# Optimization experiments

Measured on AMD Instinct MI355X. Metric: run time of the kernel, lower is better.

Reference implementation:

```python
import jax, jax.numpy as jnp
import numpy as np

N, E, G = 50000, 640000, 16384
F_IN, H = 128, 128
EPS = 1e-5
_BN_S = 1.0 / np.sqrt(1.0 + EPS)  # BatchNorm1d eval mode: running_mean=0, running_var=1


def _forward(floats, edge_src, edge_dst, game_indices):
    (x, in_bn_g, in_bn_b, lin_W, lin_b, bn0_g, bn0_b,
     cW1, cb1, bn1_g, bn1_b, cW2, cb2, bn2_g, bn2_b, cW3, cb3, bn3_g, bn3_b,
     hW1, hb1, hbn_g, hbn_b, hW2, hb2, hW3, hb3,
     oW1, ob1, obn1_g, obn1_b, oW2, ob2, obn2_g, obn2_b, oW3, ob3) = floats
    n = x.shape[0]

    def bn(z, g, b):  # eval-mode BN with zero running mean, unit running var
        return g * (z * _BN_S) + b

    # GCN symmetric normalization with self-loops: deg_i = 1 + in_degree_i
    deg = jnp.ones((n,), x.dtype).at[edge_dst].add(1.0)
    dis = jax.lax.rsqrt(deg)
    coef = (dis[edge_src] * dis[edge_dst])[:, None]      # [E,1]
    self_coef = (dis * dis)[:, None]                      # [N,1] self-loop weight 1/deg

    def gcn(h, W, b):
        hw = h @ W                                        # [N,H]
        agg = jax.ops.segment_sum(hw[edge_src] * coef, edge_dst, num_segments=n)
        return agg + hw * self_coef + b

    h = bn(x, in_bn_g, in_bn_b)
    h = jax.nn.relu(bn(h @ lin_W + lin_b, bn0_g, bn0_b))
    h = h + jax.nn.relu(bn(gcn(h, cW1, cb1), bn1_g, bn1_b))
    h = h + jax.nn.relu(bn(gcn(h, cW2, cb2), bn2_g, bn2_b))
    h = h + jax.nn.relu(bn(gcn(h, cW3, cb3), bn3_g, bn3_b))

    xg = h[game_indices]                                  # [G,H]
    z = jnp.einsum('gf,hfo->hgo', xg, hW1) + hb1[:, None, :]
    z = jax.nn.relu(hbn_g[:, None, :] * (z * _BN_S) + hbn_b[:, None, :])
    z = jax.nn.relu(jnp.einsum('hgo,hok->hgk', z, hW2) + hb2[:, None, :])
    heads = (jnp.einsum('hgk,hko->hgo', z, hW3) + hb3[:, None, :])[:, :, 0].T  # [G,4]
    # outcome classification head -> [G,3]
    o = jax.nn.relu(bn(xg @ oW1 + ob1, obn1_g, obn1_b))
    o = jax.nn.relu(bn(o @ oW2 + ob2, obn2_g, obn2_b))
    o = o @ oW3 + ob3
    # columns: home_goals, away_goals, home_shots, away_shots, outcome_logits(3)
    return jnp.concatenate([heads, o], axis=-1)          # [G,7]


def setup_inputs() -> dict:
    key = jax.random.key(0)
    ks = iter(jax.random.split(key, 64))
    f32 = jnp.float32

    def rn(shape, s=0.05):
        return jax.random.normal(next(ks), shape, f32) * s

    H2, H4 = H // 2, H // 4
    return {
        'x': jax.random.normal(next(ks), (N, F_IN), f32),
        'edge_src': jax.random.randint(next(ks), (E,), 0, N),
        'edge_dst': jax.random.randint(next(ks), (E,), 0, N),
        'game_indices': jax.random.randint(next(ks), (G,), 0, N),
        'in_bn_g': jnp.ones((F_IN,), f32), 'in_bn_b': jnp.zeros((F_IN,), f32),
        'lin_W': rn((F_IN, H)), 'lin_b': jnp.zeros((H,), f32),
        'bn0_g': jnp.ones((H,), f32), 'bn0_b': jnp.zeros((H,), f32),
        'cW1': rn((H, H)), 'cb1': jnp.zeros((H,), f32),
        'bn1_g': jnp.ones((H,), f32), 'bn1_b': jnp.zeros((H,), f32),
        'cW2': rn((H, H)), 'cb2': jnp.zeros((H,), f32),
        'bn2_g': jnp.ones((H,), f32), 'bn2_b': jnp.zeros((H,), f32),
        'cW3': rn((H, H)), 'cb3': jnp.zeros((H,), f32),
        'bn3_g': jnp.ones((H,), f32), 'bn3_b': jnp.zeros((H,), f32),
        'hW1': rn((4, H, H2)), 'hb1': jnp.zeros((4, H2), f32),
        'hbn_g': jnp.ones((4, H2), f32), 'hbn_b': jnp.zeros((4, H2), f32),
        'hW2': rn((4, H2, H4)), 'hb2': jnp.zeros((4, H4), f32),
        'hW3': rn((4, H4, 1)), 'hb3': jnp.zeros((4, 1), f32),
        'oW1': rn((H, H2)), 'ob1': jnp.zeros((H2,), f32),
        'obn1_g': jnp.ones((H2,), f32), 'obn1_b': jnp.zeros((H2,), f32),
        'oW2': rn((H2, H4)), 'ob2': jnp.zeros((H4,), f32),
        'obn2_g': jnp.ones((H4,), f32), 'obn2_b': jnp.zeros((H4,), f32),
        'oW3': rn((H4, 3)), 'ob3': jnp.zeros((3,), f32),
    }


def reference(x, edge_src, edge_dst, game_indices, in_bn_g, in_bn_b, lin_W, lin_b,
              bn0_g, bn0_b, cW1, cb1, bn1_g, bn1_b, cW2, cb2, bn2_g, bn2_b,
              cW3, cb3, bn3_g, bn3_b, hW1, hb1, hbn_g, hbn_b, hW2, hb2, hW3, hb3,
              oW1, ob1, obn1_g, obn1_b, oW2, ob2, obn2_g, obn2_b, oW3, ob3):
    floats = (x, in_bn_g, in_bn_b, lin_W, lin_b, bn0_g, bn0_b,
              cW1, cb1, bn1_g, bn1_b, cW2, cb2, bn2_g, bn2_b, cW3, cb3, bn3_g, bn3_b,
              hW1, hb1, hbn_g, hbn_b, hW2, hb2, hW3, hb3,
              oW1, ob1, obn1_g, obn1_b, oW2, ob2, obn2_g, obn2_b, oW3, ob3)
    return _forward(floats, edge_src, edge_dst, game_indices)
```

## Files before the change

### kernel.cpp

```cpp
#include <hip/hip_runtime.h>
#include <hip/hip_bf16.h>

#define HDIM 128
static constexpr float BN_S = 0.99999500003749968751f;

typedef float f32x4 __attribute__((ext_vector_type(4)));
typedef short s16x8 __attribute__((ext_vector_type(8)));

union U128 { uint4 u; s16x8 s; };

__device__ __forceinline__ unsigned short f2bs(float f){
    union{float f; unsigned u;} c; c.f = f;
    unsigned r = c.u + 0x7fffu + ((c.u >> 16) & 1u);
    return (unsigned short)(r >> 16);
}
__device__ __forceinline__ float bs2f(unsigned short s){
    union{unsigned u; float f;} c; c.u = ((unsigned)s) << 16;
    return c.f;
}
__device__ __forceinline__ float ulo(unsigned u){ union{unsigned i; float f;} c; c.i = u << 16; return c.f; }
__device__ __forceinline__ float uhi(unsigned u){ union{unsigned i; float f;} c; c.i = u & 0xffff0000u; return c.f; }

__global__ __launch_bounds__(256) void k_prepzero(
    const float* __restrict__ linW, const float* __restrict__ cW1,
    const float* __restrict__ cW2, const float* __restrict__ cW3,
    const float* __restrict__ hW1, const float* __restrict__ oW1,
    const float* __restrict__ hW2, const float* __restrict__ oW2,
    unsigned short* __restrict__ wf, unsigned short* __restrict__ p1,
    unsigned short* __restrict__ p2, int* __restrict__ cnt, int N)
{
    int id = blockIdx.x * 256 + threadIdx.x;
    if (id < 65536){
        int mat = id >> 14;
        int el = id & 16383;
        int k = el >> 7, n = el & 127;
        const float* W = (mat == 0) ? linW : (mat == 1) ? cW1 : (mat == 2) ? cW2 : cW3;
        float v = W[k * 128 + n];
        unsigned short hs = f2bs(v);
        unsigned short ls = f2bs(v - bs2f(hs));
        int nt = n >> 4, lanen = n & 15, kc = k >> 5, quad = (k >> 3) & 3, j = k & 7;
        int lane = quad * 16 + lanen;
        size_t base = (size_t)mat * 32768;
        wf[base + (size_t)(((nt * 4 + kc) * 2 + 0) * 64 + lane) * 8 + j] = hs;
        wf[base + (size_t)(((nt * 4 + kc) * 2 + 1) * 64 + lane) * 8 + j] = ls;
    } else if (id < 65536 + 51200){
        int id1 = id - 65536;
        if (id1 < 40960){
            int j = id1 & 7, lane = (id1 >> 3) & 63, kc = (id1 >> 9) & 3, nt = (id1 >> 11) & 3, y = id1 >> 13;
            int k = kc * 32 + (lane >> 4) * 8 + j;
            int n = nt * 16 + (lane & 15);
            float w = (y < 4) ? hW1[(y * 128 + k) * 64 + n] : oW1[k * 64 + n];
            p1[id1] = f2bs(w);
        } else {
            int id2 = id1 - 40960;
            int j = id2 & 7, lane = (id2 >> 3) & 63, kc = (id2 >> 9) & 1, nt = (id2 >> 10) & 1, y = id2 >> 11;
            int k = kc * 32 + (lane >> 4) * 8 + j;
            int n = nt * 16 + (lane & 15);
            float w = (y < 4) ? hW2[(y * 64 + k) * 32 + n] : oW2[k * 32 + n];
            p2[id2] = f2bs(w);
        }
    } else {
        int z = id - (65536 + 51200);
        if (z < N) cnt[z] = 0;
    }
}

__global__ __launch_bounds__(256) void k_bsum(const int* __restrict__ cnt, int* __restrict__ bsum, int N){
    int b = blockIdx.x, t = threadIdx.x;
    int s = 0;
#pragma unroll
    for (int i = 0; i < 4; ++i){
        int idx = b * 1024 + i * 256 + t;
        if (idx < N) s += cnt[idx];
    }
    for (int off = 32; off; off >>= 1) s += __shfl_down(s, off);
    __shared__ int ws[4];
    if ((t & 63) == 0) ws[t >> 6] = s;
    __syncthreads();
    if (t == 0) bsum[b] = ws[0] + ws[1] + ws[2] + ws[3];
}

__global__ __launch_bounds__(256) void k_bscan(const int* __restrict__ bsum, int* __restrict__ bpre,
                                               int* __restrict__ rowptr, int B, int N, int E){
    __shared__ int arr[256];
    int t = threadIdx.x;
    int v = (t < B) ? bsum[t] : 0;
    arr[t] = v;
    for (int off = 1; off < 256; off <<= 1){
        __syncthreads();
        int x = (t >= off) ? arr[t - off] : 0;
        __syncthreads();
        arr[t] += x;
    }
    __syncthreads();
    if (t < B) bpre[t] = arr[t] - v;
    if (t == 0) rowptr[N] = E;
}

__global__ __launch_bounds__(1024) void k_scan3(const int* __restrict__ cnt, const int* __restrict__ bpre,
                                                int* __restrict__ rowptr, float* __restrict__ dis, int N){
    __shared__ int arr[1024];
    int b = blockIdx.x, t = threadIdx.x;
    int idx = b * 1024 + t;
    int c = (idx < N) ? cnt[idx] : 0;
    arr[t] = c;
    for (int off = 1; off < 1024; off <<= 1){
        __syncthreads();
        int x = (t >= off) ? arr[t - off] : 0;
        __syncthreads();
        arr[t] += x;
    }
    __syncthreads();
    if (idx < N){
        rowptr[idx] = bpre[b] + arr[t] - c;
        dis[idx] = rsqrtf(1.0f + (float)c);
    }
}

__device__ __forceinline__ void gemm01_tile(
    int tile, const float* __restrict__ A,
    const uint4* __restrict__ wf0, const uint4* __restrict__ wf1,
    const float* __restrict__ ing, const float* __restrict__ inb,
    const float* __restrict__ ebias, const float* __restrict__ eg, const float* __restrict__ eb,
    float* __restrict__ hout, unsigned short* __restrict__ hwout, int nrows,
    unsigned* sbuf)
{
    unsigned* sAhi = sbuf;
    unsigned* sAlo = sbuf + 64 * 68;
    int t = threadIdx.x;
    int row0 = tile * 64;
    for (int i = t; i < 2048; i += 256){
        int r = i >> 5, q = i & 31;
        int gr = row0 + r;
        float4 v = make_float4(0.f, 0.f, 0.f, 0.f);
        if (gr < nrows) v = *(const float4*)&A[(size_t)gr * 128 + q * 4];
        float4 g = *(const float4*)&ing[q * 4];
        float4 bo = *(const float4*)&inb[q * 4];
        v.x = v.x * (g.x * BN_S) + bo.x;
        v.y = v.y * (g.y * BN_S) + bo.y;
        v.z = v.z * (g.z * BN_S) + bo.z;
        v.w = v.w * (g.w * BN_S) + bo.w;
        unsigned u0 = __float_as_uint(v.x), u1 = __float_as_uint(v.y);
        unsigned u2 = __float_as_uint(v.z), u3 = __float_as_uint(v.w);
        uint2 hi = make_uint2((u0 >> 16) | (u1 & 0xffff0000u), (u2 >> 16) | (u3 & 0xffff0000u));
        unsigned short l0 = f2bs(v.x - __uint_as_float(u0 & 0xffff0000u));
        unsigned short l1 = f2bs(v.y - __uint_as_float(u1 & 0xffff0000u));
        unsigned short l2 = f2bs(v.z - __uint_as_float(u2 & 0xffff0000u));
        unsigned short l3 = f2bs(v.w - __uint_as_float(u3 & 0xffff0000u));
        uint2 lo = make_uint2((unsigned)l0 | ((unsigned)l1 << 16), (unsigned)l2 | ((unsigned)l3 << 16));
        *(uint2*)&sAhi[r * 68 + q * 2] = hi;
        *(uint2*)&sAlo[r * 68 + q * 2] = lo;
    }
    __syncthreads();

    int w = t >> 6, l = t & 63;
    int lanen = l & 15, quad = l >> 4;
    int mrow = w * 16 + lanen;
    f32x4 acc[8];
#pragma unroll
    for (int i = 0; i < 8; ++i) acc[i] = (f32x4){0.f, 0.f, 0.f, 0.f};

#pragma unroll 1
    for (int kc = 0; kc < 4; ++kc){
        U128 ahi, alo;
        ahi.u = *(const uint4*)&sAhi[mrow * 68 + kc * 16 + quad * 4];
        alo.u = *(const uint4*)&sAlo[mrow * 68 + kc * 16 + quad * 4];
        U128 whi[8];
#pragma unroll
        for (int nt = 0; nt < 8; ++nt)
            whi[nt].u = wf0[((nt * 4 + kc) * 2 + 0) * 64 + l];
#pragma unroll
        for (int nt = 0; nt < 8; ++nt)
            acc[nt] = __builtin_amdgcn_mfma_f32_16x16x32_bf16(ahi.s, whi[nt].s, acc[nt], 0, 0, 0);
#pragma unroll
        for (int nt = 0; nt < 8; ++nt)
            acc[nt] = __builtin_amdgcn_mfma_f32_16x16x32_bf16(alo.s, whi[nt].s, acc[nt], 0, 0, 0);
    }

    __syncthreads();
    float* so = (float*)sbuf;
#pragma unroll
    for (int nt = 0; nt < 8; ++nt){
        int n = nt * 16 + lanen;
        float bias = ebias[n], g = eg[n], bo = eb[n];
#pragma unroll
        for (int r = 0; r < 4; ++r){
            int row = w * 16 + quad * 4 + r;
            float v = g * ((acc[nt][r] + bias) * BN_S) + bo;
            so[row * 132 + n] = fmaxf(v, 0.f);
        }
    }
    __syncthreads();
    for (int i = t; i < 2048; i += 256){
        int row = i >> 5, c4 = (i & 31) * 4;
        int grow = row0 + row;
        if (grow < nrows)
            *(float4*)&hout[(size_t)grow * 128 + c4] = *(float4*)&so[row * 132 + c4];
    }

    f32x4 acc2[8];
#pragma unroll
    for (int i = 0; i < 8; ++i) acc2[i] = (f32x4){0.f, 0.f, 0.f, 0.f};
#pragma unroll 1
    for (int kc = 0; kc < 4; ++kc){
        float4 a0 = *(const float4*)&so[mrow * 132 + kc * 32 + quad * 8];
        float4 a1 = *(const float4*)&so[mrow * 132 + kc * 32 + quad * 8 + 4];
        U128 af;
        af.u.x = (unsigned)f2bs(a0.x) | ((unsigned)f2bs(a0.y) << 16);
        af.u.y = (unsigned)f2bs(a0.z) | ((unsigned)f2bs(a0.w) << 16);
        af.u.z = (unsigned)f2bs(a1.x) | ((unsigned)f2bs(a1.y) << 16);
        af.u.w = (unsigned)f2bs(a1.z) | ((unsigned)f2bs(a1.w) << 16);
        U128 wh[8];
#pragma unroll
        for (int nt = 0; nt < 8; ++nt)
            wh[nt].u = wf1[((nt * 4 + kc) * 2 + 0) * 64 + l];
#pragma unroll
        for (int nt = 0; nt < 8; ++nt)
            acc2[nt] = __builtin_amdgcn_mfma_f32_16x16x32_bf16(af.s, wh[nt].s, acc2[nt], 0, 0, 0);
    }
    __syncthreads();
    unsigned short* ss = (unsigned short*)sbuf;
#pragma unroll
    for (int nt = 0; nt < 8; ++nt){
        int n = nt * 16 + lanen;
#pragma unroll
        for (int r = 0; r < 4; ++r){
            int row = w * 16 + quad * 4 + r;
            ss[row * 136 + n] = f2bs(acc2[nt][r]);
        }
    }
    __syncthreads();
    for (int i = t; i < 1024; i += 256){
        int row = i >> 4, c = i & 15;
        int grow = row0 + row;
        if (grow < nrows)
            *(uint4*)&hwout[(size_t)grow * 128 + c * 8] = *(uint4*)&ss[row * 136 + c * 8];
    }
}

__global__ __launch_bounds__(256) void k_cg01(
    const float* __restrict__ x, const uint4* __restrict__ wf0, const uint4* __restrict__ wf1,
    const float* __restrict__ ing, const float* __restrict__ inb,
    const float* __restrict__ lb, const float* __restrict__ g0, const float* __restrict__ b0,
    float* __restrict__ hbuf, unsigned short* __restrict__ hwb, int nrows, int gb,
    const int* __restrict__ edst, int* __restrict__ cnt, int* __restrict__ rank, int E)
{
    __shared__ __align__(16) unsigned sbuf[64 * 136];
    int bid = blockIdx.x;
    if (bid < gb){
        gemm01_tile(bid, x, wf0, wf1, ing, inb, lb, g0, b0, hbuf, hwb, nrows, sbuf);
    } else {
        int base = (bid - gb) * 1024;
#pragma unroll
        for (int ii = 0; ii < 4; ++ii){
            int e = base + ii * 256 + threadIdx.x;
            if (e < E){
                int r = atomicAdd(&cnt[edst[e]], 1);
                rank[e] = r;
            }
        }
    }
}

__global__ __launch_bounds__(256) void k_fill(
    const int* __restrict__ esrc, const int* __restrict__ edst,
    const int* __restrict__ rowptr, const int* __restrict__ rank,
    const float* __restrict__ dis, int2* __restrict__ ipk, int E)
{
    int base = blockIdx.x * 1024;
#pragma unroll
    for (int ii = 0; ii < 4; ++ii){
        int e = base + ii * 256 + threadIdx.x;
        if (e < E){
            int s = esrc[e], d = edst[e];
            ipk[rowptr[d] + rank[e]] = make_int2(s, __float_as_int(dis[s]));
        }
    }
}

__global__ __launch_bounds__(256) void k_gemmb(
    const uint4* __restrict__ hb16, const uint4* __restrict__ wf,
    unsigned short* __restrict__ hwout, int nrows)
{
    __shared__ __align__(16) unsigned sbuf[64 * 68];
    int t = threadIdx.x;
    int row0 = blockIdx.x * 64;
    for (int i = t; i < 1024; i += 256){
        int r = i >> 4, c = i & 15;
        int gr = row0 + r;
        uint4 v = make_uint4(0u, 0u, 0u, 0u);
        if (gr < nrows) v = hb16[(size_t)gr * 16 + c];
        *(uint4*)&sbuf[r * 68 + c * 4] = v;
    }
    __syncthreads();

    int w = t >> 6, l = t & 63;
    int lanen = l & 15, quad = l >> 4;
    int mrow = w * 16 + lanen;
    f32x4 acc[8];
#pragma unroll
    for (int i = 0; i < 8; ++i) acc[i] = (f32x4){0.f, 0.f, 0.f, 0.f};
#pragma unroll 1
    for (int kc = 0; kc < 4; ++kc){
        U128 ah;
        ah.u = *(const uint4*)&sbuf[mrow * 68 + kc * 16 + quad * 4];
        U128 wh[8];
#pragma unroll
        for (int nt = 0; nt < 8; ++nt)
            wh[nt].u = wf[((nt * 4 + kc) * 2 + 0) * 64 + l];
#pragma unroll
        for (int nt = 0; nt < 8; ++nt)
            acc[nt] = __builtin_amdgcn_mfma_f32_16x16x32_bf16(ah.s, wh[nt].s, acc[nt], 0, 0, 0);
    }
    __syncthreads();
    unsigned short* ss = (unsigned short*)sbuf;
#pragma unroll
    for (int nt = 0; nt < 8; ++nt){
        int n = nt * 16 + lanen;
#pragma unroll
        for (int r = 0; r < 4; ++r){
            int row = w * 16 + quad * 4 + r;
            ss[row * 136 + n] = f2bs(acc[nt][r]);
        }
    }
    __syncthreads();
    for (int i = t; i < 1024; i += 256){
        int row = i >> 4, c = i & 15;
        int grow = row0 + row;
        if (grow < nrows)
            *(uint4*)&hwout[(size_t)grow * 128 + c * 8] = *(uint4*)&ss[row * 136 + c * 8];
    }
}

__global__ __launch_bounds__(256) void k_agg(
    const unsigned* __restrict__ hwu, float* __restrict__ h,
    const int* __restrict__ rowptr, const int2* __restrict__ ipk,
    const float* __restrict__ dis,
    const float* __restrict__ cb, const float* __restrict__ bg, const float* __restrict__ bb,
    uint4* __restrict__ hb16o, int N)
{
    int row = blockIdx.x * 4 + (threadIdx.x >> 6);
    if (row >= N) return;
    int l = threadIdx.x & 63;
    int sub = l >> 4, cg = l & 15;
    int b = rowptr[row], e = rowptr[row + 1];
    float acc[8];
#pragma unroll
    for (int i = 0; i < 8; ++i) acc[i] = 0.f;
    for (int p = b; p < e; p += 16){
        int base = p + sub * 4;
        if (base < e){
            int2 i0 = ipk[base];
            int2 i1 = (base + 1 < e) ? ipk[base + 1] : make_int2(i0.x, 0);
            int2 i2 = (base + 2 < e) ? ipk[base + 2] : make_int2(i0.x, 0);
            int2 i3 = (base + 3 < e) ? ipk[base + 3] : make_int2(i0.x, 0);
            uint4 v0 = *(const uint4*)&hwu[(size_t)i0.x * 64 + cg * 4];
            uint4 v1 = *(const uint4*)&hwu[(size_t)i1.x * 64 + cg * 4];
            uint4 v2 = *(const uint4*)&hwu[(size_t)i2.x * 64 + cg * 4];
            uint4 v3 = *(const uint4*)&hwu[(size_t)i3.x * 64 + cg * 4];
            float c0 = __int_as_float(i0.y), c1 = __int_as_float(i1.y);
            float c2 = __int_as_float(i2.y), c3 = __int_as_float(i3.y);
            acc[0] = fmaf(ulo(v0.x), c0, acc[0]); acc[1] = fmaf(uhi(v0.x), c0, acc[1]);
            acc[2] = fmaf(ulo(v0.y), c0, acc[2]); acc[3] = fmaf(uhi(v0.y), c0, acc[3]);
            acc[4] = fmaf(ulo(v0.z), c0, acc[4]); acc[5] = fmaf(uhi(v0.z), c0, acc[5]);
            acc[6] = fmaf(ulo(v0.w), c0, acc[6]); acc[7] = fmaf(uhi(v0.w), c0, acc[7]);
            acc[0] = fmaf(ulo(v1.x), c1, acc[0]); acc[1] = fmaf(uhi(v1.x), c1, acc[1]);
            acc[2] = fmaf(ulo(v1.y), c1, acc[2]); acc[3] = fmaf(uhi(v1.y), c1, acc[3]);
            acc[4] = fmaf(ulo(v1.z), c1, acc[4]); acc[5] = fmaf(uhi(v1.z), c1, acc[5]);
            acc[6] = fmaf(ulo(v1.w), c1, acc[6]); acc[7] = fmaf(uhi(v1.w), c1, acc[7]);
            acc[0] = fmaf(ulo(v2.x), c2, acc[0]); acc[1] = fmaf(uhi(v2.x), c2, acc[1]);
            acc[2] = fmaf(ulo(v2.y), c2, acc[2]); acc[3] = fmaf(uhi(v2.y), c2, acc[3]);
            acc[4] = fmaf(ulo(v2.z), c2, acc[4]); acc[5] = fmaf(uhi(v2.z), c2, acc[5]);
            acc[6] = fmaf(ulo(v2.w), c2, acc[6]); acc[7] = fmaf(uhi(v2.w), c2, acc[7]);
            acc[0] = fmaf(ulo(v3.x), c3, acc[0]); acc[1] = fmaf(uhi(v3.x), c3, acc[1]);
            acc[2] = fmaf(ulo(v3.y), c3, acc[2]); acc[3] = fmaf(uhi(v3.y), c3, acc[3]);
            acc[4] = fmaf(ulo(v3.z), c3, acc[4]); acc[5] = fmaf(uhi(v3.z), c3, acc[5]);
            acc[6] = fmaf(ulo(v3.w), c3, acc[6]); acc[7] = fmaf(uhi(v3.w), c3, acc[7]);
        }
    }
#pragma unroll
    for (int i = 0; i < 8; ++i){
        acc[i] += __shfl_xor(acc[i], 16);
        acc[i] += __shfl_xor(acc[i], 32);
    }
    if (sub == 0){
        float d = dis[row];
        float dd = d * d;
        uint4 sv = *(const uint4*)&hwu[(size_t)row * 64 + cg * 4];
        float sf[8] = {ulo(sv.x), uhi(sv.x), ulo(sv.y), uhi(sv.y),
                       ulo(sv.z), uhi(sv.z), ulo(sv.w), uhi(sv.w)};
        float4 c0 = *(const float4*)&cb[cg * 8], c1 = *(const float4*)&cb[cg * 8 + 4];
        float4 g0 = *(const float4*)&bg[cg * 8], g1 = *(const float4*)&bg[cg * 8 + 4];
        float4 b0 = *(const float4*)&bb[cg * 8], b1 = *(const float4*)&bb[cg * 8 + 4];
        float cc[8] = {c0.x, c0.y, c0.z, c0.w, c1.x, c1.y, c1.z, c1.w};
        float gg[8] = {g0.x, g0.y, g0.z, g0.w, g1.x, g1.y, g1.z, g1.w};
        float bo[8] = {b0.x, b0.y, b0.z, b0.w, b1.x, b1.y, b1.z, b1.w};
        float4 cur0 = *(float4*)&h[(size_t)row * 128 + cg * 8];
        float4 cur1 = *(float4*)&h[(size_t)row * 128 + cg * 8 + 4];
        float o[8] = {cur0.x, cur0.y, cur0.z, cur0.w, cur1.x, cur1.y, cur1.z, cur1.w};
#pragma unroll
        for (int i = 0; i < 8; ++i){
            float v = gg[i] * ((acc[i] * d + sf[i] * dd + cc[i]) * BN_S) + bo[i];
            o[i] += fmaxf(v, 0.f);
        }
        *(float4*)&h[(size_t)row * 128 + cg * 8] = make_float4(o[0], o[1], o[2], o[3]);
        *(float4*)&h[(size_t)row * 128 + cg * 8 + 4] = make_float4(o[4], o[5], o[6], o[7]);
        uint4 pk;
        pk.x = (unsigned)f2bs(o[0]) | ((unsigned)f2bs(o[1]) << 16);
        pk.y = (unsigned)f2bs(o[2]) | ((unsigned)f2bs(o[3]) << 16);
        pk.z = (unsigned)f2bs(o[4]) | ((unsigned)f2bs(o[5]) << 16);
        pk.w = (unsigned)f2bs(o[6]) | ((unsigned)f2bs(o[7]) << 16);
        hb16o[(size_t)row * 16 + cg] = pk;
    }
}

__global__ __launch_bounds__(256) void k_headmm(
    const uint4* __restrict__ hb16, const int* __restrict__ gidx,
    const uint4* __restrict__ p1v, const uint4* __restrict__ p2v,
    const float* __restrict__ hb1, const float* __restrict__ hg1, const float* __restrict__ hbb1,
    const float* __restrict__ hb2,
    const float* __restrict__ hW3, const float* __restrict__ hb3,
    const float* __restrict__ ob1, const float* __restrict__ og1, const float* __restrict__ obb1,
    const float* __restrict__ ob2, const float* __restrict__ og2, const float* __restrict__ obb2,
    const float* __restrict__ oW3, const float* __restrict__ ob3,
    float* __restrict__ out, int G)
{
    __shared__ __align__(16) unsigned sxg[64 * 68];
    __shared__ __align__(16) unsigned sz1u[64 * 36];
    __shared__ __align__(16) unsigned sz2u[64 * 20];
    __shared__ float sb1[64], sg1[64], sbb1[64];
    __shared__ float sb2[32], sg2[32], sbb2[32];
    __shared__ float sW3[96];
    __shared__ float sb3[3];
    __shared__ int sgi[64];

    int t = threadIdx.x;
    int gblk = blockIdx.x;
    int w = t >> 6, l = t & 63;
    int lanen = l & 15, quad = l >> 4;

    if (t < 64){
        int g = gblk * 64 + t;
        sgi[t] = (g < G) ? gidx[g] : 0;
    }
    __syncthreads();
    for (int i = t; i < 1024; i += 256){
        int r = i >> 4, c = i & 15;
        int node = sgi[r];
        uint4 v = hb16[(size_t)node * 16 + c];
        *(uint4*)&sxg[r * 68 + c * 4] = v;
    }

    for (int y = 0; y < 5; ++y){
        bool bn2 = (y == 4);
        const float* b1  = bn2 ? ob1  : (hb1 + y * 64);
        const float* g1  = bn2 ? og1  : (hg1 + y * 64);
        const float* bb1 = bn2 ? obb1 : (hbb1 + y * 64);
        const float* b2  = bn2 ? ob2  : (hb2 + y * 32);
        const float* W3  = bn2 ? oW3  : (hW3 + y * 32);
        const float* b3  = bn2 ? ob3  : (hb3 + y);
        int nc3 = bn2 ? 3 : 1;

        __syncthreads();
        if (t < 64){
            sb1[t] = b1[t]; sg1[t] = g1[t]; sbb1[t] = bb1[t];
            if (t < 3) sb3[t] = (t < nc3) ? b3[t] : 0.f;
        } else if (t < 96){
            int p = t - 64;
            sb2[p] = b2[p];
            sg2[p] = bn2 ? og2[p] : 1.f;
            sbb2[p] = bn2 ? obb2[p] : 0.f;
        } else if (t < 192){
            int i = t - 96;
            sW3[i] = (i < 32 * nc3) ? W3[i] : 0.f;
        }
        __syncthreads();

        f32x4 acc1[4] = {{0.f,0.f,0.f,0.f},{0.f,0.f,0.f,0.f},{0.f,0.f,0.f,0.f},{0.f,0.f,0.f,0.f}};
#pragma unroll
        for (int kc = 0; kc < 4; ++kc){
            U128 a;
            a.u = *(const uint4*)&sxg[(w * 16 + lanen) * 68 + kc * 16 + quad * 4];
#pragma unroll
            for (int nt = 0; nt < 4; ++nt){
                U128 bfr;
                bfr.u = p1v[((y * 4 + nt) * 4 + kc) * 64 + l];
                acc1[nt] = __builtin_amdgcn_mfma_f32_16x16x32_bf16(a.s, bfr.s, acc1[nt], 0, 0, 0);
            }
        }
        {
            unsigned short* sz1s = (unsigned short*)sz1u;
#pragma unroll
            for (int nt = 0; nt < 4; ++nt){
                int n = nt * 16 + lanen;
                float g = sg1[n], bia = sb1[n], bt = sbb1[n];
#pragma unroll
                for (int r = 0; r < 4; ++r){
                    int row = w * 16 + quad * 4 + r;
                    float v = g * ((acc1[nt][r] + bia) * BN_S) + bt;
                    sz1s[row * 72 + n] = f2bs(fmaxf(v, 0.f));
                }
            }
        }
        __syncthreads();

        f32x4 acc2[2] = {{0.f,0.f,0.f,0.f},{0.f,0.f,0.f,0.f}};
#pragma unroll
        for (int kc = 0; kc < 2; ++kc){
            U128 a;
            a.u = *(const uint4*)&sz1u[(w * 16 + lanen) * 36 + kc * 16 + quad * 4];
#pragma unroll
            for (int nt = 0; nt < 2; ++nt){
                U128 bfr;
                bfr.u = p2v[((y * 2 + nt) * 2 + kc) * 64 + l];
                acc2[nt] = __builtin_amdgcn_mfma_f32_16x16x32_bf16(a.s, bfr.s, acc2[nt], 0, 0, 0);
            }
        }
        {
            unsigned short* sz2s = (unsigned short*)sz2u;
#pragma unroll
            for (int nt = 0; nt < 2; ++nt){
                int n = nt * 16 + lanen;
                float bia = sb2[n], g = sg2[n], bt = sbb2[n];
#pragma unroll
                for (int r = 0; r < 4; ++r){
                    int row = w * 16 + quad * 4 + r;
                    float v = acc2[nt][r] + bia;
                    if (bn2) v = g * (v * BN_S) + bt;
                    sz2s[row * 40 + n] = f2bs(fmaxf(v, 0.f));
                }
            }
        }
        __syncthreads();

        const unsigned short* sz2s = (const unsigned short*)sz2u;
        if (!bn2){
            if (t < 64){
                int g = gblk * 64 + t;
                if (g < G){
                    float s = sb3[0];
#pragma unroll
                    for (int p = 0; p < 32; ++p) s = fmaf(bs2f(sz2s[t * 40 + p]), sW3[p], s);
                    out[(size_t)g * 7 + y] = s;
                }
            }
        } else {
            if (t < 192){
                int gl = t / 3, c = t % 3;
                int g = gblk * 64 + gl;
                if (g < G){
                    float s = sb3[c];
#pragma unroll
                    for (int p = 0; p < 32; ++p) s = fmaf(bs2f(sz2s[gl * 40 + p]), sW3[p * 3 + c], s);
                    out[(size_t)g * 7 + 4 + c] = s;
                }
            }
        }
    }
}

extern "C" void kernel_launch(void* const* d_in, const int* in_sizes, int n_in,
                              void* d_out, int out_size, void* d_ws, size_t ws_size,
                              hipStream_t stream)
{
    const float* x    = (const float*)d_in[0];
    const int* esrc   = (const int*)d_in[1];
    const int* edst   = (const int*)d_in[2];
    const int* gidx   = (const int*)d_in[3];
    const float* in_g = (const float*)d_in[4];
    const float* in_b = (const float*)d_in[5];
    const float* lin_W = (const float*)d_in[6];
    const float* lin_b = (const float*)d_in[7];
    const float* bn0_g = (const float*)d_in[8];
    const float* bn0_b = (const float*)d_in[9];
    const float* cW[3] = {(const float*)d_in[10], (const float*)d_in[14], (const float*)d_in[18]};
    const float* cb[3] = {(const float*)d_in[11], (const float*)d_in[15], (const float*)d_in[19]};
    const float* bg[3] = {(const float*)d_in[12], (const float*)d_in[16], (const float*)d_in[20]};
    const float* bb[3] = {(const float*)d_in[13], (const float*)d_in[17], (const float*)d_in[21]};
    const float* hW1 = (const float*)d_in[22];
    const float* hb1 = (const float*)d_in[23];
    const float* hg1 = (const float*)d_in[24];
    const float* hbb1 = (const float*)d_in[25];
    const float* hW2 = (const float*)d_in[26];
    const float* hb2 = (const float*)d_in[27];
    const float* hW3 = (const float*)d_in[28];
    const float* hb3 = (const float*)d_in[29];
    const float* oW1 = (const float*)d_in[30];
    const float* ob1 = (const float*)d_in[31];
    const float* og1 = (const float*)d_in[32];
    const float* obb1 = (const float*)d_in[33];
    const float* oW2 = (const float*)d_in[34];
    const float* ob2 = (const float*)d_in[35];
    const float* og2 = (const float*)d_in[36];
    const float* obb2 = (const float*)d_in[37];
    const float* oW3 = (const float*)d_in[38];
    const float* ob3 = (const float*)d_in[39];

    const int N = in_sizes[0] / HDIM;
    const int E = in_sizes[1];
    const int G = in_sizes[3];

    char* wsp = (char*)d_ws;
    size_t off = 0;
    auto alloc = [&](size_t bytes) -> char* {
        char* p = wsp + off;
        off = (off + bytes + 255) & ~(size_t)255;
        return p;
    };
    float* dis    = (float*)alloc((size_t)N * 4);
    int* rowptr   = (int*)alloc((size_t)(N + 1) * 4);
    int* cnt      = (int*)alloc((size_t)N * 4);
    int* rank     = (int*)alloc((size_t)E * 4);
    int2* ipk     = (int2*)alloc((size_t)E * 8);
    float* hbuf   = (float*)alloc((size_t)N * HDIM * 4);
    unsigned short* hwb = (unsigned short*)alloc((size_t)N * HDIM * 2);
    unsigned short* hb16 = (unsigned short*)alloc((size_t)N * HDIM * 2);
    unsigned short* p1 = (unsigned short*)alloc(40960 * 2);
    unsigned short* p2 = (unsigned short*)alloc(10240 * 2);
    unsigned short* wf = (unsigned short*)alloc((size_t)4 * 32768 * 2);
    int* bsum     = (int*)alloc(256 * 4);
    int* bpre     = (int*)alloc(256 * 4);

    int gb = (N + 63) / 64;
    int CB = (E + 1023) / 1024;
    int B = (N + 1023) / 1024;
    int prepTot = 65536 + 51200 + N;

    k_prepzero<<<dim3((prepTot + 255) / 256), dim3(256), 0, stream>>>(
        lin_W, cW[0], cW[1], cW[2], hW1, oW1, hW2, oW2, wf, p1, p2, cnt, N);
    k_cg01<<<dim3(gb + CB), dim3(256), 0, stream>>>(
        x, (const uint4*)wf, (const uint4*)(wf + (size_t)32768),
        in_g, in_b, lin_b, bn0_g, bn0_b, hbuf, hwb, N, gb, edst, cnt, rank, E);
    k_bsum<<<dim3(B), dim3(256), 0, stream>>>(cnt, bsum, N);
    k_bscan<<<dim3(1), dim3(256), 0, stream>>>(bsum, bpre, rowptr, B, N, E);
    k_scan3<<<dim3(B), dim3(1024), 0, stream>>>(cnt, bpre, rowptr, dis, N);
    k_fill<<<dim3(CB), dim3(256), 0, stream>>>(esrc, edst, rowptr, rank, dis, ipk, E);
    k_agg<<<dim3((N + 3) / 4), dim3(256), 0, stream>>>((const unsigned*)hwb, hbuf, rowptr, ipk,
                                                       dis, cb[0], bg[0], bb[0], (uint4*)hb16, N);
    for (int lyr = 1; lyr < 3; ++lyr){
        k_gemmb<<<dim3(gb), dim3(256), 0, stream>>>((const uint4*)hb16,
                                                    (const uint4*)(wf + (size_t)(1 + lyr) * 32768),
                                                    hwb, N);
        k_agg<<<dim3((N + 3) / 4), dim3(256), 0, stream>>>((const unsigned*)hwb, hbuf, rowptr, ipk,
                                                           dis, cb[lyr], bg[lyr], bb[lyr], (uint4*)hb16, N);
    }
    k_headmm<<<dim3((G + 63) / 64), dim3(256), 0, stream>>>(
        (const uint4*)hb16, gidx, (const uint4*)p1, (const uint4*)p2,
        hb1, hg1, hbb1, hb2, hW3, hb3,
        ob1, og1, obb1, ob2, og2, obb2, oW3, ob3,
        (float*)d_out, G);
}
```

Measured before the change: 364.1 us.

## Fuse GCN aggregation with next layer's GEMM via shared memory, ping-pong hw buffers

The aggregation for layers 1 and 2 now runs inside a combined kernel that keeps each 64-row block's bf16 output in shared memory and immediately multiplies it by the next layer's weights with MFMA. This removes the round trip of hb16 through global memory and two kernel launches. Because the gather reads hw while the kernel writes the next hw, two ping-pong buffers are used. The final layer's aggregation no longer writes the fp32 residual buffer, since nothing reads it afterwards. The trade-off is lower parallelism: one block now handles 64 rows instead of 4, with each wave processing 16 rows serially, which can worsen latency hiding and load balance on skewed degrees.

```diff
diff --git a/kernel.cpp b/kernel.cpp
--- a/kernel.cpp
+++ b/kernel.cpp
@@ -278,24 +278,102 @@
     }
 }
 
-__global__ __launch_bounds__(256) void k_gemmb(
-    const uint4* __restrict__ hb16, const uint4* __restrict__ wf,
-    unsigned short* __restrict__ hwout, int nrows)
+__global__ __launch_bounds__(256) void k_aggemm(
+    const unsigned* __restrict__ hwu, float* __restrict__ h,
+    const int* __restrict__ rowptr, const int2* __restrict__ ipk,
+    const float* __restrict__ dis,
+    const float* __restrict__ cb, const float* __restrict__ bg, const float* __restrict__ bb,
+    const uint4* __restrict__ wf, unsigned short* __restrict__ hwout, int N)
 {
     __shared__ __align__(16) unsigned sbuf[64 * 68];
     int t = threadIdx.x;
+    int w = t >> 6, l = t & 63;
+    int sub = l >> 4, cg = l & 15;
+    int lanen = l & 15, quad = l >> 4;
     int row0 = blockIdx.x * 64;
-    for (int i = t; i < 1024; i += 256){
-        int r = i >> 4, c = i & 15;
-        int gr = row0 + r;
-        uint4 v = make_uint4(0u, 0u, 0u, 0u);
-        if (gr < nrows) v = hb16[(size_t)gr * 16 + c];
-        *(uint4*)&sbuf[r * 68 + c * 4] = v;
-    }
-    __syncthreads();
-
-    int w = t >> 6, l = t & 63;
-    int lanen = l & 15, quad = l >> 4;
+
+    if (row0 + 64 > N){
+        for (int i = t; i < 1024; i += 256){
+            int r = i >> 4;
+            if (row0 + r >= N) *(uint4*)&sbuf[r * 68 + (i & 15) * 4] = make_uint4(0u,0u,0u,0u);
+        }
+    }
+
+    for (int rr = 0; rr < 16; ++rr){
+        int row = row0 + w * 16 + rr;
+        if (row >= N) break;
+        int b = rowptr[row], e = rowptr[row + 1];
+        float acc[8];
+#pragma unroll
+        for (int i = 0; i < 8; ++i) acc[i] = 0.f;
+        for (int p = b; p < e; p += 16){
+            int base = p + sub * 4;
+            if (base < e){
+                int2 i0 = ipk[base];
+                int2 i1 = (base + 1 < e) ? ipk[base + 1] : make_int2(i0.x, 0);
+                int2 i2 = (base + 2 < e) ? ipk[base + 2] : make_int2(i0.x, 0);
+                int2 i3 = (base + 3 < e) ? ipk[base + 3] : make_int2(i0.x, 0);
+                uint4 v0 = *(const uint4*)&hwu[(size_t)i0.x * 64 + cg * 4];
+                uint4 v1 = *(const uint4*)&hwu[(size_t)i1.x * 64 + cg * 4];
+                uint4 v2 = *(const uint4*)&hwu[(size_t)i2.x * 64 + cg * 4];
+                uint4 v3 = *(const uint4*)&hwu[(size_t)i3.x * 64 + cg * 4];
+                float c0 = __int_as_float(i0.y), c1 = __int_as_float(i1.y);
+                float c2 = __int_as_float(i2.y), c3 = __int_as_float(i3.y);
+                acc[0] = fmaf(ulo(v0.x), c0, acc[0]); acc[1] = fmaf(uhi(v0.x), c0, acc[1]);
+                acc[2] = fmaf(ulo(v0.y), c0, acc[2]); acc[3] = fmaf(uhi(v0.y), c0, acc[3]);
+                acc[4] = fmaf(ulo(v0.z), c0, acc[4]); acc[5] = fmaf(uhi(v0.z), c0, acc[5]);
+                acc[6] = fmaf(ulo(v0.w), c0, acc[6]); acc[7] = fmaf(uhi(v0.w), c0, acc[7]);
+                acc[0] = fmaf(ulo(v1.x), c1, acc[0]); acc[1] = fmaf(uhi(v1.x), c1, acc[1]);
+                acc[2] = fmaf(ulo(v1.y), c1, acc[2]); acc[3] = fmaf(uhi(v1.y), c1, acc[3]);
+                acc[4] = fmaf(ulo(v1.z), c1, acc[4]); acc[5] = fmaf(uhi(v1.z), c1, acc[5]);
+                acc[6] = fmaf(ulo(v1.w), c1, acc[6]); acc[7] = fmaf(uhi(v1.w), c1, acc[7]);
+                acc[0] = fmaf(ulo(v2.x), c2, acc[0]); acc[1] = fmaf(uhi(v2.x), c2, acc[1]);
+                acc[2] = fmaf(ulo(v2.y), c2, acc[2]); acc[3] = fmaf(uhi(v2.y), c2, acc[3]);
+                acc[4] = fmaf(ulo(v2.z), c2, acc[4]); acc[5] = fmaf(uhi(v2.z), c2, acc[5]);
+                acc[6] = fmaf(ulo(v2.w), c2, acc[6]); acc[7] = fmaf(uhi(v2.w), c2, acc[7]);
+                acc[0] = fmaf(ulo(v3.x), c3, acc[0]); acc[1] = fmaf(uhi(v3.x), c3, acc[1]);
+                acc[2] = fmaf(ulo(v3.y), c3, acc[2]); acc[3] = fmaf(uhi(v3.y), c3, acc[3]);
+                acc[4] = fmaf(ulo(v3.z), c3, acc[4]); acc[5] = fmaf(uhi(v3.z), c3, acc[5]);
+                acc[6] = fmaf(ulo(v3.w), c3, acc[6]); acc[7] = fmaf(uhi(v3.w), c3, acc[7]);
+            }
+        }
+#pragma unroll
+        for (int i = 0; i < 8; ++i){
+            acc[i] += __shfl_xor(acc[i], 16);
+            acc[i] += __shfl_xor(acc[i], 32);
+        }
+        if (sub == 0){
+            float d = dis[row];
+            float dd = d * d;
+            uint4 sv = *(const uint4*)&hwu[(size_t)row * 64 + cg * 4];
+            float sf[8] = {ulo(sv.x), uhi(sv.x), ulo(sv.y), uhi(sv.y),
+                           ulo(sv.z), uhi(sv.z), ulo(sv.w), uhi(sv.w)};
+            float4 c0 = *(const float4*)&cb[cg * 8], c1 = *(const float4*)&cb[cg * 8 + 4];
+            float4 g0 = *(const float4*)&bg[cg * 8], g1 = *(const float4*)&bg[cg * 8 + 4];
+            float4 b0 = *(const float4*)&bb[cg * 8], b1 = *(const float4*)&bb[cg * 8 + 4];
+            float cc[8] = {c0.x, c0.y, c0.z, c0.w, c1.x, c1.y, c1.z, c1.w};
+            float gg[8] = {g0.x, g0.y, g0.z, g0.w, g1.x, g1.y, g1.z, g1.w};
+            float bo[8] = {b0.x, b0.y, b0.z, b0.w, b1.x, b1.y, b1.z, b1.w};
+            float4 cur0 = *(float4*)&h[(size_t)row * 128 + cg * 8];
+            float4 cur1 = *(float4*)&h[(size_t)row * 128 + cg * 8 + 4];
+            float o[8] = {cur0.x, cur0.y, cur0.z, cur0.w, cur1.x, cur1.y, cur1.z, cur1.w};
+#pragma unroll
+            for (int i = 0; i < 8; ++i){
+                float v = gg[i] * ((acc[i] * d + sf[i] * dd + cc[i]) * BN_S) + bo[i];
+                o[i] += fmaxf(v, 0.f);
+            }
+            *(float4*)&h[(size_t)row * 128 + cg * 8] = make_float4(o[0], o[1], o[2], o[3]);
+            *(float4*)&h[(size_t)row * 128 + cg * 8 + 4] = make_float4(o[4], o[5], o[6], o[7]);
+            uint4 pk;
+            pk.x = (unsigned)f2bs(o[0]) | ((unsigned)f2bs(o[1]) << 16);
+            pk.y = (unsigned)f2bs(o[2]) | ((unsigned)f2bs(o[3]) << 16);
+            pk.z = (unsigned)f2bs(o[4]) | ((unsigned)f2bs(o[5]) << 16);
+            pk.w = (unsigned)f2bs(o[6]) | ((unsigned)f2bs(o[7]) << 16);
+            *(uint4*)&sbuf[(w * 16 + rr) * 68 + cg * 4] = pk;
+        }
+    }
+    __syncthreads();
+
     int mrow = w * 16 + lanen;
     f32x4 acc[8];
 #pragma unroll
@@ -327,13 +405,13 @@
     for (int i = t; i < 1024; i += 256){
         int row = i >> 4, c = i & 15;
         int grow = row0 + row;
-        if (grow < nrows)
+        if (grow < N)
             *(uint4*)&hwout[(size_t)grow * 128 + c * 8] = *(uint4*)&ss[row * 136 + c * 8];
     }
 }
 
-__global__ __launch_bounds__(256) void k_agg(
-    const unsigned* __restrict__ hwu, float* __restrict__ h,
+__global__ __launch_bounds__(256) void k_agg3(
+    const unsigned* __restrict__ hwu, const float* __restrict__ h,
     const int* __restrict__ rowptr, const int2* __restrict__ ipk,
     const float* __restrict__ dis,
     const float* __restrict__ cb, const float* __restrict__ bg, const float* __restrict__ bb,
@@ -395,16 +473,14 @@
         float cc[8] = {c0.x, c0.y, c0.z, c0.w, c1.x, c1.y, c1.z, c1.w};
         float gg[8] = {g0.x, g0.y, g0.z, g0.w, g1.x, g1.y, g1.z, g1.w};
         float bo[8] = {b0.x, b0.y, b0.z, b0.w, b1.x, b1.y, b1.z, b1.w};
-        float4 cur0 = *(float4*)&h[(size_t)row * 128 + cg * 8];
-        float4 cur1 = *(float4*)&h[(size_t)row * 128 + cg * 8 + 4];
+        float4 cur0 = *(const float4*)&h[(size_t)row * 128 + cg * 8];
+        float4 cur1 = *(const float4*)&h[(size_t)row * 128 + cg * 8 + 4];
         float o[8] = {cur0.x, cur0.y, cur0.z, cur0.w, cur1.x, cur1.y, cur1.z, cur1.w};
 #pragma unroll
         for (int i = 0; i < 8; ++i){
             float v = gg[i] * ((acc[i] * d + sf[i] * dd + cc[i]) * BN_S) + bo[i];
             o[i] += fmaxf(v, 0.f);
         }
-        *(float4*)&h[(size_t)row * 128 + cg * 8] = make_float4(o[0], o[1], o[2], o[3]);
-        *(float4*)&h[(size_t)row * 128 + cg * 8 + 4] = make_float4(o[4], o[5], o[6], o[7]);
         uint4 pk;
         pk.x = (unsigned)f2bs(o[0]) | ((unsigned)f2bs(o[1]) << 16);
         pk.y = (unsigned)f2bs(o[2]) | ((unsigned)f2bs(o[3]) << 16);
@@ -613,7 +689,8 @@
     int* rank     = (int*)alloc((size_t)E * 4);
     int2* ipk     = (int2*)alloc((size_t)E * 8);
     float* hbuf   = (float*)alloc((size_t)N * HDIM * 4);
-    unsigned short* hwb = (unsigned short*)alloc((size_t)N * HDIM * 2);
+    unsigned short* hwbA = (unsigned short*)alloc((size_t)N * HDIM * 2);
+    unsigned short* hwbB = (unsigned short*)alloc((size_t)N * HDIM * 2);
     unsigned short* hb16 = (unsigned short*)alloc((size_t)N * HDIM * 2);
     unsigned short* p1 = (unsigned short*)alloc(40960 * 2);
     unsigned short* p2 = (unsigned short*)alloc(10240 * 2);
@@ -630,20 +707,20 @@
         lin_W, cW[0], cW[1], cW[2], hW1, oW1, hW2, oW2, wf, p1, p2, cnt, N);
     k_cg01<<<dim3(gb + CB), dim3(256), 0, stream>>>(
         x, (const uint4*)wf, (const uint4*)(wf + (size_t)32768),
-        in_g, in_b, lin_b, bn0_g, bn0_b, hbuf, hwb, N, gb, edst, cnt, rank, E);
+        in_g, in_b, lin_b, bn0_g, bn0_b, hbuf, hwbA, N, gb, edst, cnt, rank, E);
     k_bsum<<<dim3(B), dim3(256), 0, stream>>>(cnt, bsum, N);
     k_bscan<<<dim3(1), dim3(256), 0, stream>>>(bsum, bpre, rowptr, B, N, E);
     k_scan3<<<dim3(B), dim3(1024), 0, stream>>>(cnt, bpre, rowptr, dis, N);
     k_fill<<<dim3(CB), dim3(256), 0, stream>>>(esrc, edst, rowptr, rank, dis, ipk, E);
-    k_agg<<<dim3((N + 3) / 4), dim3(256), 0, stream>>>((const unsigned*)hwb, hbuf, rowptr, ipk,
-                                                       dis, cb[0], bg[0], bb[0], (uint4*)hb16, N);
-    for (int lyr = 1; lyr < 3; ++lyr){
-        k_gemmb<<<dim3(gb), dim3(256), 0, stream>>>((const uint4*)hb16,
-                                                    (const uint4*)(wf + (size_t)(1 + lyr) * 32768),
-                                                    hwb, N);
-        k_agg<<<dim3((N + 3) / 4), dim3(256), 0, stream>>>((const unsigned*)hwb, hbuf, rowptr, ipk,
-                                                           dis, cb[lyr], bg[lyr], bb[lyr], (uint4*)hb16, N);
-    }
+    k_aggemm<<<dim3(gb), dim3(256), 0, stream>>>(
+        (const unsigned*)hwbA, hbuf, rowptr, ipk, dis, cb[0], bg[0], bb[0],
+        (const uint4*)(wf + (size_t)2 * 32768), hwbB, N);
+    k_aggemm<<<dim3(gb), dim3(256), 0, stream>>>(
+        (const unsigned*)hwbB, hbuf, rowptr, ipk, dis, cb[1], bg[1], bb[1],
+        (const uint4*)(wf + (size_t)3 * 32768), hwbA, N);
+    k_agg3<<<dim3((N + 3) / 4), dim3(256), 0, stream>>>(
+        (const unsigned*)hwbA, hbuf, rowptr, ipk, dis, cb[2], bg[2], bb[2],
+        (uint4*)hb16, N);
     k_headmm<<<dim3((G + 63) / 64), dim3(256), 0, stream>>>(
         (const uint4*)hb16, gidx, (const uint4*)p1, (const uint4*)p2,
         hb1, hg1, hbb1, hb2, hW3, hb3,
```

Result: slower. 379.2 us (+4.2%).
